# Kernel tuning notes

Hardware: AMD Instinct MI355X
Metric: run time of the kernel (lower is better)

## Reference

```python
import jax, jax.numpy as jnp
import numpy as np

TOP_K = 2

def setup_inputs() -> dict:
    key = jax.random.key(0)
    k1, k2, k3, k4 = jax.random.split(key, 4)
    T, H, I, E = 8192, 2048, 4096, 8
    s = 0.02
    return {
        "hidden_states": jax.random.normal(k1, (T, H), dtype=jnp.float32),
        "router_w": jax.random.normal(k2, (E, H), dtype=jnp.float32) * s,
        "ws": jax.random.normal(k3, (E, 2 * I, H), dtype=jnp.float32) * s,  # [gate; up]
        "w2s": jax.random.normal(k4, (E, H, I), dtype=jnp.float32) * s,
    }

def reference(hidden_states, router_w, ws, w2s):
    # Router gating: softmax over experts, top-k, NO renormalization
    logits = hidden_states @ router_w.T              # [T, E]
    probs = jax.nn.softmax(logits, axis=-1)
    topv, topi = jax.lax.top_k(probs, TOP_K)         # [T, K]
    T, E = probs.shape
    I = w2s.shape[2]
    # Dense routing-weight matrix [T, E]; top_k indices are unique per token
    w = jnp.zeros_like(probs).at[jnp.arange(T)[:, None], topi].set(topv)
    out = jnp.zeros_like(hidden_states)
    for e in range(E):  # fixed small expert loop; avoids [T,E,2I] blowup
        gate = hidden_states @ ws[e, :I].T           # [T, I]
        up = hidden_states @ ws[e, I:].T             # [T, I]
        h = jax.nn.silu(gate) * up                   # SwiGLU
        out = out + w[:, e:e + 1] * (h @ w2s[e].T)   # combine
    return out
```

## Files before the change

### kernel.cpp

```cpp
#include <hip/hip_runtime.h>
#include <cstdint>
#include <cstddef>

#define T_TOK 8192
#define HDIM  2048
#define IDIM  4096
#define NEXP  8
#define MAXT  72

typedef __bf16 bf16x8 __attribute__((ext_vector_type(8)));
typedef float  f32x4  __attribute__((ext_vector_type(4)));

#define BARRIER() __builtin_amdgcn_s_barrier()
#define LGKM0()   do { asm volatile("s_waitcnt lgkmcnt(0)" ::: "memory"); __builtin_amdgcn_sched_barrier(0); } while (0)
#define VMW(n)    do { asm volatile("s_waitcnt vmcnt(" #n ")" ::: "memory"); } while (0)
#define PRIO1()   __builtin_amdgcn_s_setprio(1)
#define PRIO0()   __builtin_amdgcn_s_setprio(0)

__device__ __forceinline__ unsigned short f2bf(float f) {
    union { float f; unsigned u; } v; v.f = f;
    unsigned r = v.u + 0x7FFFu + ((v.u >> 16) & 1u);
    return (unsigned short)(r >> 16);
}

__device__ __forceinline__ void gload16(const void* g, void* l) {
    __builtin_amdgcn_global_load_lds((__attribute__((address_space(1))) void*)g,
                                     (__attribute__((address_space(3))) void*)l,
                                     16, 0, 0);
}

__global__ __launch_bounds__(256) void router_k(const float* __restrict__ hs,
                                                const float* __restrict__ rw,
                                                float* __restrict__ wgt,
                                                int* __restrict__ counts,
                                                int* __restrict__ lists) {
    int gid  = blockIdx.x * 256 + threadIdx.x;
    int tok  = gid >> 6;
    int lane = threadIdx.x & 63;
    const float* x = hs + (size_t)tok * HDIM;

    float acc[NEXP];
#pragma unroll
    for (int e = 0; e < NEXP; ++e) acc[e] = 0.f;
    for (int h = lane; h < HDIM; h += 64) {
        float xv = x[h];
#pragma unroll
        for (int e = 0; e < NEXP; ++e) acc[e] = fmaf(xv, rw[e * HDIM + h], acc[e]);
    }
#pragma unroll
    for (int off = 32; off > 0; off >>= 1) {
#pragma unroll
        for (int e = 0; e < NEXP; ++e) acc[e] += __shfl_xor(acc[e], off, 64);
    }
    if (lane == 0) {
        float m = acc[0];
#pragma unroll
        for (int e = 1; e < NEXP; ++e) m = fmaxf(m, acc[e]);
        float p[NEXP]; float s = 0.f;
#pragma unroll
        for (int e = 0; e < NEXP; ++e) { p[e] = expf(acc[e] - m); s += p[e]; }
        float inv = 1.f / s;
        int i1 = 0;
#pragma unroll
        for (int e = 1; e < NEXP; ++e) if (acc[e] > acc[i1]) i1 = e;
        int i2 = -1;
#pragma unroll
        for (int e = 0; e < NEXP; ++e) if (e != i1 && (i2 < 0 || acc[e] > acc[i2])) i2 = e;
#pragma unroll
        for (int e = 0; e < NEXP; ++e)
            wgt[(size_t)tok * NEXP + e] = (e == i1 || e == i2) ? p[e] * inv : 0.f;
        int p1 = atomicAdd(&counts[i1], 1);
        lists[i1 * T_TOK + p1] = tok;
        int p2 = atomicAdd(&counts[i2], 1);
        lists[i2 * T_TOK + p2] = (1 << 16) | tok;
    }
}

__global__ void plan_k(const int* __restrict__ counts, int* __restrict__ offs,
                       int* __restrict__ desc, int* __restrict__ ntiles) {
    if (threadIdx.x == 0 && blockIdx.x == 0) {
        int off = 0, n = 0;
        for (int e = 0; e < NEXP; ++e) {
            offs[e] = off;
            int nt = (counts[e] + 255) >> 8;
            for (int t = 0; t < nt; ++t) desc[n++] = (e << 16) | t;
            off += nt * 256;
        }
        *ntiles = n;
    }
}

__global__ __launch_bounds__(256) void cvt_k(const float* __restrict__ in,
                                             unsigned short* __restrict__ out, long n4) {
    long i      = (long)blockIdx.x * 256 + threadIdx.x;
    long stride = (long)gridDim.x * 256;
    const float4* in4 = (const float4*)in;
    ushort4* out4 = (ushort4*)out;
    for (long j = i; j < n4; j += stride) {
        float4 v = in4[j];
        ushort4 o;
        o.x = f2bf(v.x); o.y = f2bf(v.y); o.z = f2bf(v.z); o.w = f2bf(v.w);
        out4[j] = o;
    }
}

__global__ __launch_bounds__(512, 2) void gemm1_k(const unsigned short* __restrict__ A,
                                                  const unsigned short* __restrict__ Wall,
                                                  unsigned short* __restrict__ Hout,
                                                  const int* __restrict__ lists,
                                                  const int* __restrict__ counts,
                                                  const int* __restrict__ offs,
                                                  const int* __restrict__ desc,
                                                  const int* __restrict__ ntiles) {
    const int slot = blockIdx.y;
    if (slot >= *ntiles) return;
    const int dsc = desc[slot];
    const int e = dsc >> 16, tt = dsc & 0xFFFF;
    const int cnt = counts[e];
    const int t0 = tt * 256;
    const int* list = lists + e * T_TOK;
    const unsigned short* W = Wall + (size_t)e * 2 * IDIM * HDIM;
    const int hbase = offs[e];
    const int n0 = blockIdx.x * 128;

    extern __shared__ __align__(16) char lds[];

    const int tid  = threadIdx.x;
    const int lane = tid & 63;
    const int wid  = tid >> 6;
    const int wr   = wid >> 2;
    const int wc   = wid & 3;

    const int prow = tid >> 3;
    const int pcol = (tid & 7) * 16;
    const int lcol = (pcol ^ ((prow & 7) << 4)) >> 1;
    unsigned aoff[4];
#pragma unroll
    for (int i = 0; i < 4; ++i) {
        int g = t0 + i * 64 + prow;
        int tok = list[(g < cnt) ? g : t0] & 0xFFFF;
        aoff[i] = (unsigned)tok * HDIM + lcol;
    }
    unsigned goff[2], uoff[2];
#pragma unroll
    for (int i = 0; i < 2; ++i) {
        goff[i] = (unsigned)(n0 + i * 64 + prow) * HDIM + lcol;
        uoff[i] = (unsigned)(IDIM + n0 + i * 64 + prow) * HDIM + lcol;
    }
    const int dst = tid * 16;

#define SG_AH0(b, t) do { unsigned k0_ = (unsigned)((t) & 31) * 64;      \
    gload16(A + aoff[0] + k0_, lds + (b) * 32768 + dst);                 \
    gload16(A + aoff[1] + k0_, lds + (b) * 32768 + 8192 + dst); } while (0)
#define SG_AH1(b, t) do { unsigned k0_ = (unsigned)((t) & 31) * 64;      \
    gload16(A + aoff[2] + k0_, lds + (b) * 32768 + 16384 + dst);         \
    gload16(A + aoff[3] + k0_, lds + (b) * 32768 + 24576 + dst); } while (0)
#define SG_G(b, t) do { unsigned k0_ = (unsigned)((t) & 31) * 64;        \
    gload16(W + goff[0] + k0_, lds + 65536 + (b) * 16384 + dst);         \
    gload16(W + goff[1] + k0_, lds + 65536 + (b) * 16384 + 8192 + dst); } while (0)
#define SG_U(b, t) do { unsigned k0_ = (unsigned)((t) & 31) * 64;        \
    gload16(W + uoff[0] + k0_, lds + 98304 + (b) * 16384 + dst);         \
    gload16(W + uoff[1] + k0_, lds + 98304 + (b) * 16384 + 8192 + dst); } while (0)

    const int frd = (lane & 7) << 4;
    const int cb0 = (((lane >> 4) * 16)     ) ^ frd;
    const int cb1 = (((lane >> 4) * 16) | 64) ^ frd;
    const int arow = (wr * 64 + (lane & 15)) * 128;
    const int brow = (wc * 32 + (lane & 15)) * 128;

    f32x4 accg[8][2], accu[8][2];
#pragma unroll
    for (int mi = 0; mi < 8; ++mi)
#pragma unroll
        for (int ni = 0; ni < 2; ++ni) {
            accg[mi][ni] = (f32x4){0.f, 0.f, 0.f, 0.f};
            accu[mi][ni] = (f32x4){0.f, 0.f, 0.f, 0.f};
        }

    SG_AH0(0, 0); SG_AH1(0, 0); SG_G(0, 0); SG_U(0, 0);
    SG_AH0(1, 1); SG_AH1(1, 1); SG_G(1, 1); SG_U(1, 1);
    VMW(0);
    BARRIER();

    const int NT = HDIM / 64;
    for (int kt = 0; kt < NT; ++kt) {
        const int b  = kt & 1;
        const int bn = b ^ 1;
        const char* la = lds + b * 32768 + arow;
        const char* lg = lds + 65536 + b * 16384 + brow;
        const char* lu = lds + 98304 + b * 16384 + brow;
        bf16x8 a0[2][4], bg[2][2], bu[2][2];

        VMW(6);
#pragma unroll
        for (int mi = 0; mi < 4; ++mi) {
            a0[0][mi] = *(const bf16x8*)(la + mi * 2048 + cb0);
            a0[1][mi] = *(const bf16x8*)(la + mi * 2048 + cb1);
        }
#pragma unroll
        for (int ni = 0; ni < 2; ++ni) {
            bg[0][ni] = *(const bf16x8*)(lg + ni * 2048 + cb0);
            bg[1][ni] = *(const bf16x8*)(lg + ni * 2048 + cb1);
        }
        SG_AH1(bn, kt + 1);
        BARRIER(); LGKM0(); PRIO1();
#pragma unroll
        for (int ks = 0; ks < 2; ++ks)
#pragma unroll
            for (int mi = 0; mi < 4; ++mi)
#pragma unroll
                for (int ni = 0; ni < 2; ++ni)
                    accg[mi][ni] = __builtin_amdgcn_mfma_f32_16x16x32_bf16(a0[ks][mi], bg[ks][ni], accg[mi][ni], 0, 0, 0);
        PRIO0(); BARRIER();

        VMW(6);
#pragma unroll
        for (int ni = 0; ni < 2; ++ni) {
            bu[0][ni] = *(const bf16x8*)(lu + ni * 2048 + cb0);
            bu[1][ni] = *(const bf16x8*)(lu + ni * 2048 + cb1);
        }
        SG_U(bn, kt + 1);
        BARRIER(); LGKM0(); PRIO1();
#pragma unroll
        for (int ks = 0; ks < 2; ++ks)
#pragma unroll
            for (int mi = 0; mi < 4; ++mi)
#pragma unroll
                for (int ni = 0; ni < 2; ++ni)
                    accu[mi][ni] = __builtin_amdgcn_mfma_f32_16x16x32_bf16(a0[ks][mi], bu[ks][ni], accu[mi][ni], 0, 0, 0);
        PRIO0(); BARRIER();

        VMW(6);
#pragma unroll
        for (int mi = 0; mi < 4; ++mi) {
            a0[0][mi] = *(const bf16x8*)(la + 16384 + mi * 2048 + cb0);
            a0[1][mi] = *(const bf16x8*)(la + 16384 + mi * 2048 + cb1);
        }
        SG_AH0(b, kt + 2);
        BARRIER(); LGKM0(); PRIO1();
#pragma unroll
        for (int ks = 0; ks < 2; ++ks)
#pragma unroll
            for (int mi = 0; mi < 4; ++mi)
#pragma unroll
                for (int ni = 0; ni < 2; ++ni)
                    accg[mi + 4][ni] = __builtin_amdgcn_mfma_f32_16x16x32_bf16(a0[ks][mi], bg[ks][ni], accg[mi + 4][ni], 0, 0, 0);
        PRIO0(); BARRIER();

        SG_G(b, kt + 2);
        PRIO1();
#pragma unroll
        for (int ks = 0; ks < 2; ++ks)
#pragma unroll
            for (int mi = 0; mi < 4; ++mi)
#pragma unroll
                for (int ni = 0; ni < 2; ++ni)
                    accu[mi + 4][ni] = __builtin_amdgcn_mfma_f32_16x16x32_bf16(a0[ks][mi], bu[ks][ni], accu[mi + 4][ni], 0, 0, 0);
        PRIO0(); BARRIER();
    }
    VMW(0);
#undef SG_AH0
#undef SG_AH1
#undef SG_G
#undef SG_U

#pragma unroll
    for (int mi = 0; mi < 8; ++mi)
#pragma unroll
        for (int ni = 0; ni < 2; ++ni)
#pragma unroll
            for (int j = 0; j < 4; ++j) {
                int qr = mi >> 2, m = mi & 3;
                int row = hbase + t0 + qr * 128 + wr * 64 + m * 16 + ((lane >> 4) << 2) + j;
                int col = n0 + wc * 32 + ni * 16 + (lane & 15);
                float g = accg[mi][ni][j], u = accu[mi][ni][j];
                float hv = (g / (1.f + expf(-g))) * u;
                Hout[(size_t)row * IDIM + col] = f2bf(hv);
            }
}

__global__ __launch_bounds__(512, 4) void gemm2_k(const unsigned short* __restrict__ Ah,
                                                  const unsigned short* __restrict__ Ball,
                                                  const float* __restrict__ wgt,
                                                  float* __restrict__ outP,
                                                  const int* __restrict__ lists,
                                                  const int* __restrict__ counts,
                                                  const int* __restrict__ offs,
                                                  const int* __restrict__ desc,
                                                  const int* __restrict__ ntiles) {
    const int slot = blockIdx.y;
    if (slot >= *ntiles) return;
    const int dsc = desc[slot];
    const int e = dsc >> 16, tt = dsc & 0xFFFF;
    const int cnt = counts[e];
    const int t0 = tt * 256;
    const int* list = lists + e * T_TOK;
    const unsigned short* B = Ball + (size_t)e * HDIM * IDIM;
    const int hbase = offs[e];
    const int n0 = blockIdx.x * 128;

    __shared__ __align__(16) char lds[49152];

    const int tid  = threadIdx.x;
    const int lane = tid & 63;
    const int wid  = tid >> 6;
    const int wr   = wid >> 1;
    const int wc   = wid & 1;

    const int prow = tid >> 2;
    const int pcol = (tid & 3) * 16;
    const int lcol = (pcol ^ (((prow >> 1) & 3) << 4)) >> 1;
    const unsigned aoff0 = (unsigned)(hbase + t0 + prow) * IDIM + lcol;
    const unsigned aoff1 = (unsigned)(hbase + t0 + 128 + prow) * IDIM + lcol;
    const unsigned boff  = (unsigned)(n0 + prow) * IDIM + lcol;
    const int dst = tid * 16;

#define G2_STAGE(buf, kt) do {                                        \
    unsigned k0_ = (unsigned)(kt) * 32;                               \
    gload16(Ah + aoff0 + k0_, lds + (buf) * 16384 + dst);             \
    gload16(Ah + aoff1 + k0_, lds + (buf) * 16384 + 8192 + dst);      \
    gload16(B + boff + k0_, lds + 32768 + (buf) * 8192 + dst);        \
} while (0)

    const int cb = ((lane >> 4) << 4) ^ (((lane >> 1) & 3) << 4);
    const int arow = wr * 4096 + (lane & 15) * 64;
    const int brow = wc * 4096 + (lane & 15) * 64;

    f32x4 acc[4][4];
#pragma unroll
    for (int mi = 0; mi < 4; ++mi)
#pragma unroll
        for (int ni = 0; ni < 4; ++ni) acc[mi][ni] = (f32x4){0.f, 0.f, 0.f, 0.f};

    G2_STAGE(0, 0);
    G2_STAGE(1, 1);
    VMW(3);
    BARRIER();

    const int NT = IDIM / 32;
    int buf = 0;
    for (int kt = 0; kt < NT; ++kt) {
        const char* la = lds + buf * 16384 + arow;
        const char* lb = lds + 32768 + buf * 8192 + brow;
        bf16x8 af[4], bfr[4];
#pragma unroll
        for (int mi = 0; mi < 4; ++mi) af[mi] = *(const bf16x8*)(la + mi * 1024 + cb);
#pragma unroll
        for (int ni = 0; ni < 4; ++ni) bfr[ni] = *(const bf16x8*)(lb + ni * 1024 + cb);
        LGKM0(); PRIO1();
#pragma unroll
        for (int mi = 0; mi < 4; ++mi)
#pragma unroll
            for (int ni = 0; ni < 2; ++ni)
                acc[mi][ni] = __builtin_amdgcn_mfma_f32_16x16x32_bf16(af[mi], bfr[ni], acc[mi][ni], 0, 0, 0);
        PRIO0();
        BARRIER();
        G2_STAGE(buf, (kt + 2) & (NT - 1));
        PRIO1();
#pragma unroll
        for (int mi = 0; mi < 4; ++mi)
#pragma unroll
            for (int ni = 2; ni < 4; ++ni)
                acc[mi][ni] = __builtin_amdgcn_mfma_f32_16x16x32_bf16(af[mi], bfr[ni], acc[mi][ni], 0, 0, 0);
        PRIO0();
        VMW(3);
        BARRIER();
        buf ^= 1;
    }
    VMW(0);
#undef G2_STAGE

#pragma unroll
    for (int mi = 0; mi < 4; ++mi)
#pragma unroll
        for (int j = 0; j < 4; ++j) {
            int g = t0 + wr * 64 + mi * 16 + ((lane >> 4) << 2) + j;
            if (g < cnt) {
                int ent = list[g];
                int tok = ent & 0xFFFF;
                int sl  = ent >> 16;
                float w = wgt[(size_t)tok * NEXP + e];
                float* o = outP + (size_t)sl * T_TOK * HDIM + (size_t)tok * HDIM;
#pragma unroll
                for (int ni = 0; ni < 4; ++ni) {
                    int col = n0 + wc * 64 + ni * 16 + (lane & 15);
                    o[col] = w * acc[mi][ni][j];
                }
            }
        }
}

__global__ __launch_bounds__(256) void combine_k(const float* __restrict__ p0,
                                                 const float* __restrict__ p1,
                                                 float* __restrict__ out, long n4) {
    long i      = (long)blockIdx.x * 256 + threadIdx.x;
    long stride = (long)gridDim.x * 256;
    const float4* a4 = (const float4*)p0;
    const float4* b4 = (const float4*)p1;
    float4* o4 = (float4*)out;
    for (long j = i; j < n4; j += stride) {
        float4 a = a4[j], b = b4[j];
        o4[j] = make_float4(a.x + b.x, a.y + b.y, a.z + b.z, a.w + b.w);
    }
}

extern "C" void kernel_launch(void* const* d_in, const int* in_sizes, int n_in,
                              void* d_out, int out_size, void* d_ws, size_t ws_size,
                              hipStream_t stream) {
    const float* hs  = (const float*)d_in[0];
    const float* rw  = (const float*)d_in[1];
    const float* ws  = (const float*)d_in[2];
    const float* w2s = (const float*)d_in[3];
    float* out = (float*)d_out;

    char* wsp = (char*)d_ws;
    unsigned short* hs_bf = (unsigned short*)(wsp);
    unsigned short* w_bf  = (unsigned short*)(wsp + 33554432ULL);
    unsigned short* w2_bf = (unsigned short*)(wsp + 301989888ULL);
    unsigned short* h_bf  = (unsigned short*)(wsp + 436207616ULL);
    float*          outP  = (float*)(wsp + 587202560ULL);
    float*          wgt   = (float*)(wsp + 721420288ULL);
    int*            counts = (int*)(wsp + 721682432ULL);
    int*            offs   = (int*)(wsp + 721682560ULL);
    int*            lists  = (int*)(wsp + 721682688ULL);
    int*            desc   = (int*)(wsp + 721944832ULL);
    int*            ntiles = (int*)(wsp + 721945344ULL);

    hipMemsetAsync(counts, 0, NEXP * sizeof(int), stream);
    cvt_k<<<2048, 256, 0, stream>>>(hs, hs_bf, (long)T_TOK * HDIM / 4);
    cvt_k<<<4096, 256, 0, stream>>>(ws, w_bf, (long)NEXP * 2 * IDIM * HDIM / 4);
    cvt_k<<<4096, 256, 0, stream>>>(w2s, w2_bf, (long)NEXP * HDIM * IDIM / 4);
    router_k<<<(T_TOK * 64) / 256, 256, 0, stream>>>(hs, rw, wgt, counts, lists);
    plan_k<<<1, 64, 0, stream>>>(counts, offs, desc, ntiles);

    gemm1_k<<<dim3(IDIM / 128, MAXT), 512, 131072, stream>>>(
        hs_bf, w_bf, h_bf, lists, counts, offs, desc, ntiles);
    gemm2_k<<<dim3(HDIM / 128, MAXT), 512, 0, stream>>>(
        h_bf, w2_bf, wgt, outP, lists, counts, offs, desc, ntiles);
    combine_k<<<2048, 256, 0, stream>>>(outP, outP + (size_t)T_TOK * HDIM, out,
                                        (long)T_TOK * HDIM / 4);
}
```

Before: 1.399 ms.

## Rework gemm2 into BK=64 four-phase pipeline and deepen gemm1 prefetch waits

The second expert GEMM moves from a BK=32 double-buffered loop with a 2x4 wave grid to a BK=64 schedule that mirrors the first GEMM. It uses a 2x4 wave layout with 8x2 accumulators per wave, 128-byte swizzled LDS rows, and staggered A-half and B prefetches placed between two MFMA phases. LDS doubles and occupancy is reduced to 2 blocks per CU. In the first GEMM, the initial prefetch issue is reordered and the vmcnt waits are moved and relaxed so more global loads stay in flight across barriers. The risks are lower occupancy and subtle pipeline wait-count correctness.

```diff
diff --git a/kernel.cpp b/kernel.cpp
--- a/kernel.cpp
+++ b/kernel.cpp
@@ -177,8 +177,8 @@
             accu[mi][ni] = (f32x4){0.f, 0.f, 0.f, 0.f};
         }
 
-    SG_AH0(0, 0); SG_AH1(0, 0); SG_G(0, 0); SG_U(0, 0);
-    SG_AH0(1, 1); SG_AH1(1, 1); SG_G(1, 1); SG_U(1, 1);
+    SG_AH0(0, 0); SG_G(0, 0); SG_U(0, 0); SG_AH1(0, 0);
+    SG_AH0(1, 1); SG_G(1, 1);
     VMW(0);
     BARRIER();
 
@@ -191,7 +191,6 @@
         const char* lu = lds + 98304 + b * 16384 + brow;
         bf16x8 a0[2][4], bg[2][2], bu[2][2];
 
-        VMW(6);
 #pragma unroll
         for (int mi = 0; mi < 4; ++mi) {
             a0[0][mi] = *(const bf16x8*)(la + mi * 2048 + cb0);
@@ -211,9 +210,10 @@
 #pragma unroll
                 for (int ni = 0; ni < 2; ++ni)
                     accg[mi][ni] = __builtin_amdgcn_mfma_f32_16x16x32_bf16(a0[ks][mi], bg[ks][ni], accg[mi][ni], 0, 0, 0);
-        PRIO0(); BARRIER();
-
+        PRIO0();
         VMW(6);
+        BARRIER();
+
 #pragma unroll
         for (int ni = 0; ni < 2; ++ni) {
             bu[0][ni] = *(const bf16x8*)(lu + ni * 2048 + cb0);
@@ -230,7 +230,6 @@
                     accu[mi][ni] = __builtin_amdgcn_mfma_f32_16x16x32_bf16(a0[ks][mi], bu[ks][ni], accu[mi][ni], 0, 0, 0);
         PRIO0(); BARRIER();
 
-        VMW(6);
 #pragma unroll
         for (int mi = 0; mi < 4; ++mi) {
             a0[0][mi] = *(const bf16x8*)(la + 16384 + mi * 2048 + cb0);
@@ -256,7 +255,9 @@
 #pragma unroll
                 for (int ni = 0; ni < 2; ++ni)
                     accu[mi + 4][ni] = __builtin_amdgcn_mfma_f32_16x16x32_bf16(a0[ks][mi], bu[ks][ni], accu[mi + 4][ni], 0, 0, 0);
-        PRIO0(); BARRIER();
+        PRIO0();
+        VMW(8);
+        BARRIER();
     }
     VMW(0);
 #undef SG_AH0
@@ -279,7 +280,7 @@
             }
 }
 
-__global__ __launch_bounds__(512, 4) void gemm2_k(const unsigned short* __restrict__ Ah,
+__global__ __launch_bounds__(512, 2) void gemm2_k(const unsigned short* __restrict__ Ah,
                                                   const unsigned short* __restrict__ Ball,
                                                   const float* __restrict__ wgt,
                                                   float* __restrict__ outP,
@@ -299,82 +300,114 @@
     const int hbase = offs[e];
     const int n0 = blockIdx.x * 128;
 
-    __shared__ __align__(16) char lds[49152];
+    __shared__ __align__(16) char lds[98304];
 
     const int tid  = threadIdx.x;
     const int lane = tid & 63;
     const int wid  = tid >> 6;
-    const int wr   = wid >> 1;
-    const int wc   = wid & 1;
-
-    const int prow = tid >> 2;
-    const int pcol = (tid & 3) * 16;
-    const int lcol = (pcol ^ (((prow >> 1) & 3) << 4)) >> 1;
-    const unsigned aoff0 = (unsigned)(hbase + t0 + prow) * IDIM + lcol;
-    const unsigned aoff1 = (unsigned)(hbase + t0 + 128 + prow) * IDIM + lcol;
-    const unsigned boff  = (unsigned)(n0 + prow) * IDIM + lcol;
+    const int wr   = wid >> 2;
+    const int wc   = wid & 3;
+
+    const int prow = tid >> 3;
+    const int pcol = (tid & 7) * 16;
+    const int lcol = (pcol ^ ((prow & 7) << 4)) >> 1;
+    unsigned aoff[4];
+#pragma unroll
+    for (int i = 0; i < 4; ++i)
+        aoff[i] = (unsigned)(hbase + t0 + i * 64 + prow) * IDIM + lcol;
+    unsigned boff[2];
+#pragma unroll
+    for (int i = 0; i < 2; ++i)
+        boff[i] = (unsigned)(n0 + i * 64 + prow) * IDIM + lcol;
     const int dst = tid * 16;
 
-#define G2_STAGE(buf, kt) do {                                        \
-    unsigned k0_ = (unsigned)(kt) * 32;                               \
-    gload16(Ah + aoff0 + k0_, lds + (buf) * 16384 + dst);             \
-    gload16(Ah + aoff1 + k0_, lds + (buf) * 16384 + 8192 + dst);      \
-    gload16(B + boff + k0_, lds + 32768 + (buf) * 8192 + dst);        \
-} while (0)
-
-    const int cb = ((lane >> 4) << 4) ^ (((lane >> 1) & 3) << 4);
-    const int arow = wr * 4096 + (lane & 15) * 64;
-    const int brow = wc * 4096 + (lane & 15) * 64;
-
-    f32x4 acc[4][4];
-#pragma unroll
-    for (int mi = 0; mi < 4; ++mi)
-#pragma unroll
-        for (int ni = 0; ni < 4; ++ni) acc[mi][ni] = (f32x4){0.f, 0.f, 0.f, 0.f};
-
-    G2_STAGE(0, 0);
-    G2_STAGE(1, 1);
-    VMW(3);
+#define SG_AH0(b, t) do { unsigned k0_ = (unsigned)((t) & 63) * 64;       \
+    gload16(Ah + aoff[0] + k0_, lds + (b) * 32768 + dst);                 \
+    gload16(Ah + aoff[1] + k0_, lds + (b) * 32768 + 8192 + dst); } while (0)
+#define SG_AH1(b, t) do { unsigned k0_ = (unsigned)((t) & 63) * 64;       \
+    gload16(Ah + aoff[2] + k0_, lds + (b) * 32768 + 16384 + dst);         \
+    gload16(Ah + aoff[3] + k0_, lds + (b) * 32768 + 24576 + dst); } while (0)
+#define SG_B(b, t) do { unsigned k0_ = (unsigned)((t) & 63) * 64;         \
+    gload16(B + boff[0] + k0_, lds + 65536 + (b) * 16384 + dst);          \
+    gload16(B + boff[1] + k0_, lds + 65536 + (b) * 16384 + 8192 + dst); } while (0)
+
+    const int frd = (lane & 7) << 4;
+    const int cb0 = (((lane >> 4) * 16)     ) ^ frd;
+    const int cb1 = (((lane >> 4) * 16) | 64) ^ frd;
+    const int arow = (wr * 64 + (lane & 15)) * 128;
+    const int brow = (wc * 32 + (lane & 15)) * 128;
+
+    f32x4 acc[8][2];
+#pragma unroll
+    for (int mi = 0; mi < 8; ++mi)
+#pragma unroll
+        for (int ni = 0; ni < 2; ++ni) acc[mi][ni] = (f32x4){0.f, 0.f, 0.f, 0.f};
+
+    SG_AH0(0, 0); SG_B(0, 0); SG_AH1(0, 0);
+    SG_AH0(1, 1);
+    VMW(0);
     BARRIER();
 
-    const int NT = IDIM / 32;
-    int buf = 0;
+    const int NT = IDIM / 64;
     for (int kt = 0; kt < NT; ++kt) {
-        const char* la = lds + buf * 16384 + arow;
-        const char* lb = lds + 32768 + buf * 8192 + brow;
-        bf16x8 af[4], bfr[4];
-#pragma unroll
-        for (int mi = 0; mi < 4; ++mi) af[mi] = *(const bf16x8*)(la + mi * 1024 + cb);
-#pragma unroll
-        for (int ni = 0; ni < 4; ++ni) bfr[ni] = *(const bf16x8*)(lb + ni * 1024 + cb);
-        LGKM0(); PRIO1();
-#pragma unroll
-        for (int mi = 0; mi < 4; ++mi)
-#pragma unroll
-            for (int ni = 0; ni < 2; ++ni)
-                acc[mi][ni] = __builtin_amdgcn_mfma_f32_16x16x32_bf16(af[mi], bfr[ni], acc[mi][ni], 0, 0, 0);
+        const int b  = kt & 1;
+        const int bn = b ^ 1;
+        const char* la = lds + b * 32768 + arow;
+        const char* lb = lds + 65536 + b * 16384 + brow;
+        bf16x8 a0[2][4], bb[2][2];
+
+#pragma unroll
+        for (int mi = 0; mi < 4; ++mi) {
+            a0[0][mi] = *(const bf16x8*)(la + mi * 2048 + cb0);
+            a0[1][mi] = *(const bf16x8*)(la + mi * 2048 + cb1);
+        }
+#pragma unroll
+        for (int ni = 0; ni < 2; ++ni) {
+            bb[0][ni] = *(const bf16x8*)(lb + ni * 2048 + cb0);
+            bb[1][ni] = *(const bf16x8*)(lb + ni * 2048 + cb1);
+        }
+        SG_AH1(bn, kt + 1);
+        SG_B(bn, kt + 1);
+        BARRIER(); LGKM0(); PRIO1();
+#pragma unroll
+        for (int ks = 0; ks < 2; ++ks)
+#pragma unroll
+            for (int mi = 0; mi < 4; ++mi)
+#pragma unroll
+                for (int ni = 0; ni < 2; ++ni)
+                    acc[mi][ni] = __builtin_amdgcn_mfma_f32_16x16x32_bf16(a0[ks][mi], bb[ks][ni], acc[mi][ni], 0, 0, 0);
+        PRIO0(); BARRIER();
+
+#pragma unroll
+        for (int mi = 0; mi < 4; ++mi) {
+            a0[0][mi] = *(const bf16x8*)(la + 16384 + mi * 2048 + cb0);
+            a0[1][mi] = *(const bf16x8*)(la + 16384 + mi * 2048 + cb1);
+        }
+        SG_AH0(b, kt + 2);
+        BARRIER(); LGKM0(); PRIO1();
+#pragma unroll
+        for (int ks = 0; ks < 2; ++ks)
+#pragma unroll
+            for (int mi = 0; mi < 4; ++mi)
+#pragma unroll
+                for (int ni = 0; ni < 2; ++ni)
+                    acc[mi + 4][ni] = __builtin_amdgcn_mfma_f32_16x16x32_bf16(a0[ks][mi], bb[ks][ni], acc[mi + 4][ni], 0, 0, 0);
         PRIO0();
+        VMW(2);
         BARRIER();
-        G2_STAGE(buf, (kt + 2) & (NT - 1));
-        PRIO1();
-#pragma unroll
-        for (int mi = 0; mi < 4; ++mi)
-#pragma unroll
-            for (int ni = 2; ni < 4; ++ni)
-                acc[mi][ni] = __builtin_amdgcn_mfma_f32_16x16x32_bf16(af[mi], bfr[ni], acc[mi][ni], 0, 0, 0);
-        PRIO0();
-        VMW(3);
-        BARRIER();
-        buf ^= 1;
     }
     VMW(0);
-#undef G2_STAGE
-
-#pragma unroll
-    for (int mi = 0; mi < 4; ++mi)
+#undef SG_AH0
+#undef SG_AH1
+#undef SG_B
+
+#pragma unroll
+    for (int mi = 0; mi < 8; ++mi) {
+        int qr = mi >> 2, m = mi & 3;
 #pragma unroll
         for (int j = 0; j < 4; ++j) {
-            int g = t0 + wr * 64 + mi * 16 + ((lane >> 4) << 2) + j;
+            int row_l = qr * 128 + wr * 64 + m * 16 + ((lane >> 4) << 2) + j;
+            int g = t0 + row_l;
             if (g < cnt) {
                 int ent = list[g];
                 int tok = ent & 0xFFFF;
@@ -382,12 +415,13 @@
                 float w = wgt[(size_t)tok * NEXP + e];
                 float* o = outP + (size_t)sl * T_TOK * HDIM + (size_t)tok * HDIM;
 #pragma unroll
-                for (int ni = 0; ni < 4; ++ni) {
-                    int col = n0 + wc * 64 + ni * 16 + (lane & 15);
+                for (int ni = 0; ni < 2; ++ni) {
+                    int col = n0 + wc * 32 + ni * 16 + (lane & 15);
                     o[col] = w * acc[mi][ni][j];
                 }
             }
         }
+    }
 }
 
 __global__ __launch_bounds__(256) void combine_k(const float* __restrict__ p0,
```

Measured after the change: 1.437 ms. +2.7%, slower.
